# Kernel tuning notes

Measured on AMD Instinct MI355X. Metric: run time of the kernel, lower is better.

Reference implementation:

```python
import jax, jax.numpy as jnp
import numpy as np

DEPTH = 64
H = 64
W = 64


def setup_inputs() -> dict:
    key = jax.random.key(0)
    k1, k2 = jax.random.split(key)
    B, J = 32, 18
    heatmap_out = jax.random.normal(k1, (B, J, DEPTH, H, W), dtype=jnp.float32)
    gt_coord = jax.random.uniform(k2, (B, J, 3), dtype=jnp.float32) * 63.0
    gt_vis = jnp.ones((B, J), dtype=jnp.float32)
    gt_have_depth = jnp.ones((B,), dtype=jnp.float32)
    return {"heatmap_out": heatmap_out, "gt_coord": gt_coord,
            "gt_vis": gt_vis, "gt_have_depth": gt_have_depth}


def soft_argmax(heatmaps, joint_num):
    B = heatmaps.shape[0]
    # softmax over the full 64*64*64 voxel grid per joint
    hm = jax.nn.softmax(heatmaps.reshape(B, joint_num, DEPTH * H * W), axis=2)
    hm = hm.reshape(B, joint_num, DEPTH, H, W)  # [b, j, z, y, x]
    rx = jnp.arange(1, W + 1, dtype=hm.dtype)
    ry = jnp.arange(1, H + 1, dtype=hm.dtype)
    rz = jnp.arange(1, DEPTH + 1, dtype=hm.dtype)
    # marginalize + expectation in a single contraction per axis
    accu_x = jnp.einsum('bjzyx,x->bj', hm, rx) - 1.0
    accu_y = jnp.einsum('bjzyx,y->bj', hm, ry) - 1.0
    accu_z = jnp.einsum('bjzyx,z->bj', hm, rz) - 1.0
    return jnp.stack((accu_x, accu_y, accu_z), axis=2)  # [b, j, 3]


def reference(heatmap_out, gt_coord, gt_vis, gt_have_depth):
    joint_num = gt_coord.shape[1]
    coord_out = soft_argmax(heatmap_out, joint_num)
    loss = jnp.abs(coord_out - gt_coord) * gt_vis[:, :, None]
    loss = (loss[:, :, 0] + loss[:, :, 1]
            + loss[:, :, 2] * gt_have_depth[:, None]) / 3.0
    return loss.mean()
```

## Files before the change

### kernel.cpp

```cpp
#include <hip/hip_runtime.h>
#include <math.h>

#define DEPTH 64
#define HH    64
#define WW    64
#define VOX   (DEPTH * HH * WW)
#define NB    32
#define NJ    18
#define NPAIR (NB * NJ)

#define BLOCKS_PER_PAIR 8
#define CHUNK   (VOX / BLOCKS_PER_PAIR)
#define THREADS 256
#define F4_PER_THREAD (CHUNK / (THREADS * 4))

__global__ __launch_bounds__(THREADS) void
jl_pass1(const float* __restrict__ hm, float* __restrict__ part)
{
    const int blk  = blockIdx.x;
    const int pair = blk / BLOCKS_PER_PAIR;
    const int sub  = blk % BLOCKS_PER_PAIR;
    const int t    = threadIdx.x;

    const float4* __restrict__ base =
        (const float4*)(hm + (size_t)pair * VOX + (size_t)sub * CHUNK);
    const int elem_base = sub * CHUNK;

    const float x0 = (float)((t * 4) & 63);

    float s = 0.f, sx = 0.f, sy = 0.f, sz = 0.f;

#pragma unroll 8
    for (int i = 0; i < F4_PER_THREAD; ++i) {
        const int vi  = i * THREADS + t;
        const float4 v = base[vi];
        const int lin = elem_base + vi * 4;
        const float y  = (float)((lin >> 6) & 63);
        const float z  = (float)(lin >> 12);

        const float e0 = __expf(v.x);
        const float e1 = __expf(v.y);
        const float e2 = __expf(v.z);
        const float e3 = __expf(v.w);
        const float es = e0 + e1 + e2 + e3;

        s  += es;
        sx += es * x0 + (e1 + 2.f * e2 + 3.f * e3);
        sy += es * y;
        sz += es * z;
    }

    for (int off = 32; off > 0; off >>= 1) {
        s  += __shfl_down(s,  off);
        sx += __shfl_down(sx, off);
        sy += __shfl_down(sy, off);
        sz += __shfl_down(sz, off);
    }

    __shared__ float ls[4], lsx[4], lsy[4], lsz[4];
    const int wv = t >> 6;
    if ((t & 63) == 0) { ls[wv] = s; lsx[wv] = sx; lsy[wv] = sy; lsz[wv] = sz; }
    __syncthreads();
    if (t == 0) {
        float S = ls[0], SX = lsx[0], SY = lsy[0], SZ = lsz[0];
#pragma unroll
        for (int w = 1; w < 4; ++w) { S += ls[w]; SX += lsx[w]; SY += lsy[w]; SZ += lsz[w]; }
        float* p = part + (size_t)blk * 4;
        p[0] = S; p[1] = SX; p[2] = SY; p[3] = SZ;
    }
}

__global__ __launch_bounds__(NPAIR) void
jl_pass2(const float* __restrict__ part,
         const float* __restrict__ gt_coord,
         const float* __restrict__ gt_vis,
         const float* __restrict__ gt_have_depth,
         float* __restrict__ out)
{
    const int p = threadIdx.x;
    float loss = 0.f;
    {
        float s = 0.f, sx = 0.f, sy = 0.f, sz = 0.f;
#pragma unroll
        for (int k = 0; k < BLOCKS_PER_PAIR; ++k) {
            const float* q = part + (size_t)(p * BLOCKS_PER_PAIR + k) * 4;
            s += q[0]; sx += q[1]; sy += q[2]; sz += q[3];
        }
        const float inv = 1.f / s;
        const float cx = sx * inv;
        const float cy = sy * inv;
        const float cz = sz * inv;

        const int b = p / NJ;
        const float gx = gt_coord[p * 3 + 0];
        const float gy = gt_coord[p * 3 + 1];
        const float gz = gt_coord[p * 3 + 2];
        const float vis = gt_vis[p];
        const float hd  = gt_have_depth[b];
        loss = vis * (fabsf(cx - gx) + fabsf(cy - gy) + fabsf(cz - gz) * hd)
             * (1.f / 3.f);
    }

    for (int off = 32; off > 0; off >>= 1)
        loss += __shfl_down(loss, off);
    __shared__ float red[NPAIR / 64];
    const int wv = threadIdx.x >> 6;
    if ((threadIdx.x & 63) == 0) red[wv] = loss;
    __syncthreads();
    if (threadIdx.x == 0) {
        float tot = 0.f;
#pragma unroll
        for (int w = 0; w < NPAIR / 64; ++w) tot += red[w];
        out[0] = tot * (1.f / (float)NPAIR);
    }
}

extern "C" void kernel_launch(void* const* d_in, const int* in_sizes, int n_in,
                              void* d_out, int out_size, void* d_ws, size_t ws_size,
                              hipStream_t stream)
{
    const float* heatmap       = (const float*)d_in[0];
    const float* gt_coord      = (const float*)d_in[1];
    const float* gt_vis       = (const float*)d_in[2];
    const float* gt_have_depth = (const float*)d_in[3];
    float* out  = (float*)d_out;
    float* part = (float*)d_ws;

    jl_pass1<<<NPAIR * BLOCKS_PER_PAIR, THREADS, 0, stream>>>(heatmap, part);
    jl_pass2<<<1, NPAIR, 0, stream>>>(part, gt_coord, gt_vis, gt_have_depth, out);
}
```

Baseline: 752.9 us.

## Double the split per pair, use nontemporal loads, and software-pipeline fully unrolled loop

```diff
diff --git a/kernel.cpp b/kernel.cpp
--- a/kernel.cpp
+++ b/kernel.cpp
@@ -9,10 +9,24 @@
 #define NJ    18
 #define NPAIR (NB * NJ)
 
-#define BLOCKS_PER_PAIR 8
+#define BLOCKS_PER_PAIR 16
 #define CHUNK   (VOX / BLOCKS_PER_PAIR)
 #define THREADS 256
 #define F4_PER_THREAD (CHUNK / (THREADS * 4))
+
+typedef float f4 __attribute__((ext_vector_type(4)));
+
+__device__ __forceinline__ f4 ntload(const f4* p) {
+#if defined(__has_builtin)
+#if __has_builtin(__builtin_nontemporal_load)
+    return __builtin_nontemporal_load(p);
+#else
+    return *p;
+#endif
+#else
+    return *p;
+#endif
+}
 
 __global__ __launch_bounds__(THREADS) void
 jl_pass1(const float* __restrict__ hm, float* __restrict__ part)
@@ -22,33 +36,55 @@
     const int sub  = blk % BLOCKS_PER_PAIR;
     const int t    = threadIdx.x;
 
-    const float4* __restrict__ base =
-        (const float4*)(hm + (size_t)pair * VOX + (size_t)sub * CHUNK);
-    const int elem_base = sub * CHUNK;
+    const f4* __restrict__ base =
+        (const f4*)(hm + (size_t)pair * VOX + (size_t)sub * CHUNK) + t;
 
-    const float x0 = (float)((t * 4) & 63);
+    const float x0  = (float)((t * 4) & 63);
+    const float fy0 = (float)(t >> 4);
+    const float fz0 = (float)(sub * 4);
 
     float s = 0.f, sx = 0.f, sy = 0.f, sz = 0.f;
 
-#pragma unroll 8
-    for (int i = 0; i < F4_PER_THREAD; ++i) {
-        const int vi  = i * THREADS + t;
-        const float4 v = base[vi];
-        const int lin = elem_base + vi * 4;
-        const float y  = (float)((lin >> 6) & 63);
-        const float z  = (float)(lin >> 12);
+#define LOADG(g, r0, r1, r2, r3)                      \
+    r0 = ntload(base + ((g)*4 + 0) * THREADS);        \
+    r1 = ntload(base + ((g)*4 + 1) * THREADS);        \
+    r2 = ntload(base + ((g)*4 + 2) * THREADS);        \
+    r3 = ntload(base + ((g)*4 + 3) * THREADS);
 
-        const float e0 = __expf(v.x);
-        const float e1 = __expf(v.y);
-        const float e2 = __expf(v.z);
-        const float e3 = __expf(v.w);
-        const float es = e0 + e1 + e2 + e3;
+#define ACC(v, fy, fz) {                                              \
+    const float e0 = __expf(v[0]);                                    \
+    const float e1 = __expf(v[1]);                                    \
+    const float e2 = __expf(v[2]);                                    \
+    const float e3 = __expf(v[3]);                                    \
+    const float es = (e0 + e1) + (e2 + e3);                           \
+    s += es;                                                          \
+    float tx = fmaf(2.f, e2, e1);                                     \
+    tx = fmaf(3.f, e3, tx);                                           \
+    sx = fmaf(es, x0, sx);                                            \
+    sx += tx;                                                         \
+    sy = fmaf(es, (fy), sy);                                          \
+    sz = fmaf(es, (fz), sz); }
 
-        s  += es;
-        sx += es * x0 + (e1 + 2.f * e2 + 3.f * e3);
-        sy += es * y;
-        sz += es * z;
-    }
+#define GRP(r0, r1, r2, r3, g) {                                      \
+    const float fz = fz0 + (float)(g);                                \
+    ACC(r0, fy0,        fz)                                           \
+    ACC(r1, fy0 + 16.f, fz)                                           \
+    ACC(r2, fy0 + 32.f, fz)                                           \
+    ACC(r3, fy0 + 48.f, fz) }
+
+    f4 a0, a1, a2, a3, b0, b1, b2, b3;
+    LOADG(0, a0, a1, a2, a3)
+    LOADG(1, b0, b1, b2, b3)
+    GRP(a0, a1, a2, a3, 0)
+    LOADG(2, a0, a1, a2, a3)
+    GRP(b0, b1, b2, b3, 1)
+    LOADG(3, b0, b1, b2, b3)
+    GRP(a0, a1, a2, a3, 2)
+    GRP(b0, b1, b2, b3, 3)
+
+#undef LOADG
+#undef ACC
+#undef GRP
 
     for (int off = 32; off > 0; off >>= 1) {
         s  += __shfl_down(s,  off);
@@ -121,7 +157,7 @@
 {
     const float* heatmap       = (const float*)d_in[0];
     const float* gt_coord      = (const float*)d_in[1];
-    const float* gt_vis       = (const float*)d_in[2];
+    const float* gt_vis        = (const float*)d_in[2];
     const float* gt_have_depth = (const float*)d_in[3];
     float* out  = (float*)d_out;
     float* part = (float*)d_ws;
```

After: 724.9 us. 1.04x faster.
